# Kernel optimization log

Measured on AMD Instinct MI355X. Metric: run time of the kernel, lower is better.

## Reference

```python
import jax, jax.numpy as jnp
import numpy as np

IN_F = 512
OUT_F = 512
ALPHA = 0.2   # LeakyReLU negative slope
NEG_INF = -9e15


def setup_inputs() -> dict:
    key = jax.random.key(0)
    k1, k2, k3, k4 = jax.random.split(key, 4)
    B, S = 8, 2048
    hidden_state = jax.random.normal(k1, (B, S, IN_F), dtype=jnp.float32)
    adjacent_matrix = jax.random.uniform(k2, (B, S, S), dtype=jnp.float32)
    # nn.Linear weight (no bias): stored as [out, in] in torch; we keep [in, out] for x @ W
    bound = 1.0 / np.sqrt(IN_F)
    W = jax.random.uniform(k3, (IN_F, OUT_F), dtype=jnp.float32, minval=-bound, maxval=bound)
    # xavier_uniform with gain=1.414 on a: shape [2*out, 1]
    a_bound = 1.414 * np.sqrt(6.0 / (2 * OUT_F + 1))
    a = jax.random.uniform(k4, (2 * OUT_F, 1), dtype=jnp.float32, minval=-a_bound, maxval=a_bound)
    return {"hidden_state": hidden_state, "adjacent_matrix": adjacent_matrix, "W": W, "a": a}


def reference(hidden_state, adjacent_matrix, W, a):
    # Wh: [B, S, out]
    Wh = jnp.einsum('bsi,io->bso', hidden_state, W)
    # additive attention: Wh1 + Wh2^T -> [B, S, S]
    Wh1 = Wh @ a[:OUT_F, :]            # [B, S, 1]
    Wh2 = Wh @ a[OUT_F:, :]            # [B, S, 1]
    e = Wh1 + jnp.swapaxes(Wh2, 1, 2)  # [B, S, S]
    e = jax.nn.leaky_relu(e, negative_slope=ALPHA)
    attention = jnp.where(adjacent_matrix > 0.5, e, NEG_INF)
    # NOTE: original softmaxes over dim=1 (the *row* index), faithfully reproduced
    attention = jax.nn.softmax(attention, axis=1)
    # dropout is identity at inference (training=False)
    h_prime = jnp.einsum('bst,bto->bso', attention, Wh)
    return jax.nn.elu(h_prime)  # concat=True path
```

## Files before the change

### kernel.cpp

```cpp
#include <hip/hip_runtime.h>
#include <hip/hip_bf16.h>
#include <stdint.h>

#define SDIM 2048
#define BDIM 8
#define FDIM 512
constexpr float ALPHA = 0.2f;

typedef __attribute__((ext_vector_type(8))) short bf16x8;
typedef __attribute__((ext_vector_type(4))) float f32x4;

__device__ __forceinline__ unsigned short f2bf(float x) {
  __hip_bfloat16 h = __float2bfloat16(x);
  return *reinterpret_cast<unsigned short*>(&h);
}

__device__ __forceinline__ void gload_lds16(const void* g, void* l) {
  __builtin_amdgcn_global_load_lds(
      (const __attribute__((address_space(1))) unsigned int*)(uintptr_t)g,
      (__attribute__((address_space(3))) unsigned int*)(uintptr_t)l,
      16, 0, 0);
}

__global__ void k0_prep(const float* __restrict__ W, const float* __restrict__ a,
                        float* __restrict__ wa, __hip_bfloat16* __restrict__ WT) {
  int i = blockIdx.x;
  int lane = threadIdx.x;
  float s1 = 0.f, s2 = 0.f;
  for (int o = lane; o < FDIM; o += 64) {
    float w = W[i * FDIM + o];
    s1 += w * a[o];
    s2 += w * a[FDIM + o];
    WT[o * FDIM + i] = __float2bfloat16(w);
  }
  #pragma unroll
  for (int off = 32; off > 0; off >>= 1) {
    s1 += __shfl_down(s1, off);
    s2 += __shfl_down(s2, off);
  }
  if (lane == 0) { wa[i] = s1; wa[FDIM + i] = s2; }
}

__global__ __launch_bounds__(256) void k1_rows(const float* __restrict__ H,
                                               const float* __restrict__ wa,
                                               float* __restrict__ Wh1, float* __restrict__ Wh2,
                                               __hip_bfloat16* __restrict__ Hb) {
  int wid = threadIdx.x >> 6, lane = threadIdx.x & 63;
  long r = (long)blockIdx.x * 4 + wid;
  const float* hr = H + r * FDIM;
  float4 v0 = ((const float4*)hr)[lane];
  float4 v1 = ((const float4*)hr)[lane + 64];
  float4 wa10 = ((const float4*)wa)[lane];
  float4 wa11 = ((const float4*)wa)[lane + 64];
  float4 wa20 = ((const float4*)(wa + FDIM))[lane];
  float4 wa21 = ((const float4*)(wa + FDIM))[lane + 64];
  float s1 = v0.x*wa10.x + v0.y*wa10.y + v0.z*wa10.z + v0.w*wa10.w
           + v1.x*wa11.x + v1.y*wa11.y + v1.z*wa11.z + v1.w*wa11.w;
  float s2 = v0.x*wa20.x + v0.y*wa20.y + v0.z*wa20.z + v0.w*wa20.w
           + v1.x*wa21.x + v1.y*wa21.y + v1.z*wa21.z + v1.w*wa21.w;
  ushort4 u0 = { f2bf(v0.x), f2bf(v0.y), f2bf(v0.z), f2bf(v0.w) };
  ushort4 u1 = { f2bf(v1.x), f2bf(v1.y), f2bf(v1.z), f2bf(v1.w) };
  ushort4* hb = (ushort4*)(Hb + r * FDIM);
  hb[lane] = u0;
  hb[lane + 64] = u1;
  #pragma unroll
  for (int off = 32; off > 0; off >>= 1) {
    s1 += __shfl_down(s1, off);
    s2 += __shfl_down(s2, off);
  }
  if (lane == 0) { Wh1[r] = s1; Wh2[r] = s2; }
}

__global__ __launch_bounds__(256) void k2_z(const float* __restrict__ adj,
                                            const float* __restrict__ Wh1,
                                            const float* __restrict__ Wh2,
                                            float* __restrict__ Zp) {
  int t = blockIdx.x * 256 + threadIdx.x;
  int b = blockIdx.y;
  int c = blockIdx.z;
  float w2 = Wh2[b * SDIM + t];
  const float* arow = adj + ((long)b * SDIM + c * 64) * SDIM + t;
  const float* w1p = Wh1 + b * SDIM + c * 64;
  float z = 0.f;
  #pragma unroll 8
  for (int s = 0; s < 64; ++s) {
    float av = arow[(long)s * SDIM];
    float e = w1p[s] + w2;
    e = e > 0.f ? e : ALPHA * e;
    float p = __expf(e);
    z += (av > 0.5f) ? p : 0.f;
  }
  Zp[(b * 32 + c) * SDIM + t] = z;
}

__global__ void k2b_rz(const float* __restrict__ Zp, float* __restrict__ rZ) {
  int idx = blockIdx.x * 256 + threadIdx.x;
  int b = idx >> 11, t = idx & 2047;
  float z = 0.f;
  #pragma unroll
  for (int c = 0; c < 32; ++c) z += Zp[(b * 32 + c) * SDIM + t];
  rZ[idx] = 1.0f / z;
}

__global__ __launch_bounds__(256) void k3_gemm(const __hip_bfloat16* __restrict__ WTm,
                                               const __hip_bfloat16* __restrict__ Hb,
                                               const float* __restrict__ rZ,
                                               __hip_bfloat16* __restrict__ VT) {
  __shared__ __align__(16) __hip_bfloat16 Asm[2][128 * 32];
  __shared__ __align__(16) __hip_bfloat16 Bsm[2][128 * 32];
  const int o0 = blockIdx.x * 128;
  const int t0 = blockIdx.y * 128;
  const int b = blockIdx.z;
  const int tid = threadIdx.x;
  const int w = tid >> 6, lane = tid & 63;
  const int wm = w >> 1, wn = w & 1;
  const int fr = lane & 15, fq = lane >> 4;
  const int lr = lane >> 2, lb = (lane & 3) * 16;

  const __hip_bfloat16* Abase = WTm + (long)o0 * FDIM;
  const __hip_bfloat16* Bbase = Hb + ((long)b * SDIM + t0) * FDIM;

  f32x4 acc[4][4] = {};

  auto stage = [&](int kk, int buf) {
    #pragma unroll
    for (int g = 0; g < 2; ++g) {
      int rbase = g * 64 + w * 16;
      int row = rbase + lr;
      gload_lds16((const char*)(Abase + (long)row * FDIM + kk * 32) + lb,
                  (char*)&Asm[buf][0] + rbase * 64);
      gload_lds16((const char*)(Bbase + (long)row * FDIM + kk * 32) + lb,
                  (char*)&Bsm[buf][0] + rbase * 64);
    }
  };

  stage(0, 0);
  __syncthreads();
  for (int kk = 0; kk < 16; ++kk) {
    int cur = kk & 1;
    if (kk < 15) stage(kk + 1, cur ^ 1);
    bf16x8 af[4], bf_[4];
    #pragma unroll
    for (int mf = 0; mf < 4; ++mf)
      af[mf] = *(const bf16x8*)((const char*)&Asm[cur][0] + (wm * 64 + mf * 16 + fr) * 64 + fq * 16);
    #pragma unroll
    for (int nf = 0; nf < 4; ++nf)
      bf_[nf] = *(const bf16x8*)((const char*)&Bsm[cur][0] + (wn * 64 + nf * 16 + fr) * 64 + fq * 16);
    #pragma unroll
    for (int mf = 0; mf < 4; ++mf)
      #pragma unroll
      for (int nf = 0; nf < 4; ++nf)
        acc[mf][nf] = __builtin_amdgcn_mfma_f32_16x16x32_bf16(af[mf], bf_[nf], acc[mf][nf], 0, 0, 0);
    __syncthreads();
  }

  #pragma unroll
  for (int nf = 0; nf < 4; ++nf) {
    int t = t0 + wn * 64 + nf * 16 + fr;
    float rz = rZ[b * SDIM + t];
    #pragma unroll
    for (int mf = 0; mf < 4; ++mf) {
      #pragma unroll
      for (int r = 0; r < 4; ++r) {
        int o = o0 + wm * 64 + mf * 16 + fq * 4 + r;
        VT[((long)(b * FDIM + o)) * SDIM + t] = __float2bfloat16(acc[mf][nf][r] * rz);
      }
    }
  }
}

__global__ __launch_bounds__(256, 2) void k4_pv(const float* __restrict__ adj,
                                                const float* __restrict__ Wh1,
                                                const float* __restrict__ Wh2,
                                                const __hip_bfloat16* __restrict__ VT,
                                                float* __restrict__ out) {
  __shared__ __align__(16) float AdjSm[3][64 * 32];
  __shared__ __align__(16) __hip_bfloat16 Psm[2][64 * 32];
  __shared__ __align__(16) float w2l[SDIM];
  const int b  = blockIdx.x;
  const int s0 = blockIdx.y * 64;
  const int ob = blockIdx.z * 256;
  const int tid = threadIdx.x;
  const int w = tid >> 6, lane = tid & 63;
  const int fr = lane & 15, fq = lane >> 4;

  const float w1 = Wh1[b * SDIM + s0 + w * 16 + fr];
  const char* adjG = (const char*)(adj + ((long)b * SDIM + s0) * SDIM);
  const char* w2G  = (const char*)(Wh2 + (long)b * SDIM);
  const __hip_bfloat16* vbase = VT + ((long)(b * FDIM + ob + w * 64 + fr)) * SDIM;

  f32x4 acc[4][4] = {};

  auto stageA = [&](int p, int slot) {
    #pragma unroll
    for (int g = 0; g < 2; ++g) {
      int row = w * 16 + g * 8 + (lane >> 3);
      gload_lds16(adjG + ((long)row * SDIM + p * 32 + (lane & 7) * 4) * 4,
                  (char*)&AdjSm[slot][0] + (w * 16 + g * 8) * 128);
    }
  };
  auto build = [&](int p, int pbuf, int slot) {
    const char* abase = (const char*)&AdjSm[slot][0] + w * 2048 + fr * 128 + fq * 32;
    float4 a0 = *(const float4*)(abase);
    float4 a1 = *(const float4*)(abase + 16);
    const float* wrow = &w2l[p * 32 + fq * 8];
    float4 q0 = *(const float4*)(wrow);
    float4 q1 = *(const float4*)(wrow + 4);
    float aa[8] = {a0.x,a0.y,a0.z,a0.w,a1.x,a1.y,a1.z,a1.w};
    float qq[8] = {q0.x,q0.y,q0.z,q0.w,q1.x,q1.y,q1.z,q1.w};
    bf16x8 pv;
    #pragma unroll
    for (int i = 0; i < 8; ++i) {
      float e = w1 + qq[i];
      e = fmaxf(e, ALPHA * e);
      float pr = (aa[i] > 0.5f) ? __expf(e) : 0.f;
      pv[i] = (short)f2bf(pr);
    }
    *(bf16x8*)((char*)&Psm[pbuf][0] + w * 1024 + lane * 16) = pv;
  };

  #pragma unroll
  for (int g = 0; g < 2; ++g)
    gload_lds16(w2G + w * 2048 + g * 1024 + lane * 16,
                (char*)w2l + w * 2048 + g * 1024);
  stageA(0, 0);
  stageA(1, 1);
  stageA(2, 2);
  asm volatile("s_waitcnt vmcnt(0)" ::: "memory");
  __syncthreads();
  build(0, 0, 0);
  asm volatile("s_waitcnt lgkmcnt(0)" ::: "memory");
  __builtin_amdgcn_sched_barrier(0);
  __builtin_amdgcn_s_barrier();

  int slotS = 0;
  int slotB = 1;
  for (int p = 0; p < 64; ++p) {
    const int cur = p & 1;
    bf16x8 vb[4];
    #pragma unroll
    for (int nf = 0; nf < 4; ++nf)
      vb[nf] = *(const bf16x8*)(vbase + (long)nf * 16 * SDIM + p * 32 + fq * 8);
    if (p <= 60) stageA(p + 3, slotS);

    bf16x8 pa[4];
    #pragma unroll
    for (int mf = 0; mf < 4; ++mf)
      pa[mf] = *(const bf16x8*)((const char*)&Psm[cur][0] + mf * 1024 + lane * 16);

    if (p <= 62) build(p + 1, cur ^ 1, slotB);
    __builtin_amdgcn_sched_barrier(0);

    #pragma unroll
    for (int mf = 0; mf < 4; ++mf)
      #pragma unroll
      for (int nf = 0; nf < 4; ++nf)
        acc[mf][nf] = __builtin_amdgcn_mfma_f32_16x16x32_bf16(pa[mf], vb[nf], acc[mf][nf], 0, 0, 0);

    asm volatile("s_waitcnt lgkmcnt(0)" ::: "memory");
    __builtin_amdgcn_sched_barrier(0);
    __builtin_amdgcn_s_barrier();

    slotS = slotB;
    slotB = (slotB == 2) ? 0 : slotB + 1;
  }

  float* orow = out + ((long)b * SDIM + s0) * FDIM + ob + w * 64;
  #pragma unroll
  for (int mf = 0; mf < 4; ++mf) {
    #pragma unroll
    for (int nf = 0; nf < 4; ++nf) {
      #pragma unroll
      for (int r = 0; r < 4; ++r) {
        int s = mf * 16 + fq * 4 + r;
        int o = nf * 16 + fr;
        float x = acc[mf][nf][r];
        x = x > 0.f ? x : (__expf(x) - 1.f);
        orow[(long)s * FDIM + o] = x;
      }
    }
  }
}

extern "C" void kernel_launch(void* const* d_in, const int* in_sizes, int n_in,
                              void* d_out, int out_size, void* d_ws, size_t ws_size,
                              hipStream_t stream) {
  const float* H   = (const float*)d_in[0];
  const float* adj = (const float*)d_in[1];
  const float* W   = (const float*)d_in[2];
  const float* a   = (const float*)d_in[3];
  float* out = (float*)d_out;
  char* ws = (char*)d_ws;

  __hip_bfloat16* VT  = (__hip_bfloat16*)(ws + 0);
  __hip_bfloat16* Hb  = (__hip_bfloat16*)(ws + 16777216);
  __hip_bfloat16* WT  = (__hip_bfloat16*)(ws + 33554432);
  float* wa  = (float*)(ws + 34078720);
  float* Wh1 = (float*)(ws + 34082816);
  float* Wh2 = (float*)(ws + 34148352);
  float* rZ  = (float*)(ws + 34213888);
  float* Zp  = (float*)(ws + 34279424);

  hipLaunchKernelGGL(k0_prep, dim3(512), dim3(64), 0, stream, W, a, wa, WT);
  hipLaunchKernelGGL(k1_rows, dim3(4096), dim3(256), 0, stream, H, wa, Wh1, Wh2, Hb);
  hipLaunchKernelGGL(k2_z, dim3(8, 8, 32), dim3(256), 0, stream, adj, Wh1, Wh2, Zp);
  hipLaunchKernelGGL(k2b_rz, dim3(64), dim3(256), 0, stream, Zp, rZ);
  hipLaunchKernelGGL(k3_gemm, dim3(4, 16, 8), dim3(256), 0, stream, WT, Hb, rZ, VT);
  hipLaunchKernelGGL(k4_pv, dim3(8, 32, 2), dim3(256), 0, stream, adj, Wh1, Wh2, VT, out);
}
```

Measured before the change: 150.3 us.

## Load adjacency directly into registers with rotating prefetch instead of LDS staging

Replaces the global-to-LDS async staging of adjacency tiles with direct per-thread float4 global loads into a four-set register rotation, prefetching three phases ahead. The main loop is unrolled by four so the register sets rotate statically. This drops the LDS round trip and frees LDS, but raises register pressure and relies on vmcnt ordering handled by the compiler. It also raises wave priority around the MFMA block with s_setprio.

```diff
diff --git a/kernel.cpp b/kernel.cpp
--- a/kernel.cpp
+++ b/kernel.cpp
@@ -174,7 +174,6 @@
                                                 const float* __restrict__ Wh2,
                                                 const __hip_bfloat16* __restrict__ VT,
                                                 float* __restrict__ out) {
-  __shared__ __align__(16) float AdjSm[3][64 * 32];
   __shared__ __align__(16) __hip_bfloat16 Psm[2][64 * 32];
   __shared__ __align__(16) float w2l[SDIM];
   const int b  = blockIdx.x;
@@ -185,25 +184,18 @@
   const int fr = lane & 15, fq = lane >> 4;
 
   const float w1 = Wh1[b * SDIM + s0 + w * 16 + fr];
-  const char* adjG = (const char*)(adj + ((long)b * SDIM + s0) * SDIM);
-  const char* w2G  = (const char*)(Wh2 + (long)b * SDIM);
+  const float* adjR = adj + ((long)(b * SDIM + s0 + w * 16 + fr)) * SDIM;
   const __hip_bfloat16* vbase = VT + ((long)(b * FDIM + ob + w * 64 + fr)) * SDIM;
 
   f32x4 acc[4][4] = {};
 
-  auto stageA = [&](int p, int slot) {
-    #pragma unroll
-    for (int g = 0; g < 2; ++g) {
-      int row = w * 16 + g * 8 + (lane >> 3);
-      gload_lds16(adjG + ((long)row * SDIM + p * 32 + (lane & 7) * 4) * 4,
-                  (char*)&AdjSm[slot][0] + (w * 16 + g * 8) * 128);
-    }
+  auto loadA = [&](int pp, float4& a0, float4& a1) {
+    const float* s = adjR + pp * 32 + fq * 8;
+    a0 = *(const float4*)s;
+    a1 = *(const float4*)(s + 4);
   };
-  auto build = [&](int p, int pbuf, int slot) {
-    const char* abase = (const char*)&AdjSm[slot][0] + w * 2048 + fr * 128 + fq * 32;
-    float4 a0 = *(const float4*)(abase);
-    float4 a1 = *(const float4*)(abase + 16);
-    const float* wrow = &w2l[p * 32 + fq * 8];
+  auto build = [&](int pp, int pbuf, const float4& a0, const float4& a1) {
+    const float* wrow = &w2l[pp * 32 + fq * 8];
     float4 q0 = *(const float4*)(wrow);
     float4 q1 = *(const float4*)(wrow + 4);
     float aa[8] = {a0.x,a0.y,a0.z,a0.w,a1.x,a1.y,a1.z,a1.w};
@@ -219,50 +211,54 @@
     *(bf16x8*)((char*)&Psm[pbuf][0] + w * 1024 + lane * 16) = pv;
   };
 
-  #pragma unroll
-  for (int g = 0; g < 2; ++g)
-    gload_lds16(w2G + w * 2048 + g * 1024 + lane * 16,
-                (char*)w2l + w * 2048 + g * 1024);
-  stageA(0, 0);
-  stageA(1, 1);
-  stageA(2, 2);
-  asm volatile("s_waitcnt vmcnt(0)" ::: "memory");
+  {
+    const float* src = Wh2 + (long)b * SDIM + tid * 8;
+    float4 t0 = *(const float4*)(src);
+    float4 t1 = *(const float4*)(src + 4);
+    *(float4*)(&w2l[tid * 8]) = t0;
+    *(float4*)(&w2l[tid * 8 + 4]) = t1;
+  }
+  float4 a0A, a1A, a0B, a1B, a0C, a1C, a0D, a1D;
+  loadA(0, a0A, a1A);
+  loadA(1, a0B, a1B);
+  loadA(2, a0C, a1C);
   __syncthreads();
-  build(0, 0, 0);
+  build(0, 0, a0A, a1A);
   asm volatile("s_waitcnt lgkmcnt(0)" ::: "memory");
   __builtin_amdgcn_sched_barrier(0);
   __builtin_amdgcn_s_barrier();
 
-  int slotS = 0;
-  int slotB = 1;
-  for (int p = 0; p < 64; ++p) {
+  auto phase = [&](int p, const float4& c0, const float4& c1, float4& f0, float4& f1) {
     const int cur = p & 1;
     bf16x8 vb[4];
     #pragma unroll
     for (int nf = 0; nf < 4; ++nf)
       vb[nf] = *(const bf16x8*)(vbase + (long)nf * 16 * SDIM + p * 32 + fq * 8);
-    if (p <= 60) stageA(p + 3, slotS);
-
+    if (p + 3 < 64) loadA(p + 3, f0, f1);
+    __builtin_amdgcn_sched_barrier(0);
     bf16x8 pa[4];
     #pragma unroll
     for (int mf = 0; mf < 4; ++mf)
       pa[mf] = *(const bf16x8*)((const char*)&Psm[cur][0] + mf * 1024 + lane * 16);
-
-    if (p <= 62) build(p + 1, cur ^ 1, slotB);
+    if (p + 1 < 64) build(p + 1, cur ^ 1, c0, c1);
     __builtin_amdgcn_sched_barrier(0);
-
+    __builtin_amdgcn_s_setprio(1);
     #pragma unroll
     for (int mf = 0; mf < 4; ++mf)
       #pragma unroll
       for (int nf = 0; nf < 4; ++nf)
         acc[mf][nf] = __builtin_amdgcn_mfma_f32_16x16x32_bf16(pa[mf], vb[nf], acc[mf][nf], 0, 0, 0);
-
+    __builtin_amdgcn_s_setprio(0);
     asm volatile("s_waitcnt lgkmcnt(0)" ::: "memory");
     __builtin_amdgcn_sched_barrier(0);
     __builtin_amdgcn_s_barrier();
-
-    slotS = slotB;
-    slotB = (slotB == 2) ? 0 : slotB + 1;
+  };
+
+  for (int j = 0; j < 16; ++j) {
+    phase(4 * j + 0, a0B, a1B, a0D, a1D);
+    phase(4 * j + 1, a0C, a1C, a0A, a1A);
+    phase(4 * j + 2, a0D, a1D, a0B, a1B);
+    phase(4 * j + 3, a0A, a1A, a0C, a1C);
   }
 
   float* orow = out + ((long)b * SDIM + s0) * FDIM + ob + w * 64;
```

Measured after the change: 148.5 us. Within noise of the previous version (-1.2%).
